# Performance work log

Hardware: AMD Instinct MI355X
Metric: run time of the kernel (lower is better)

## Reference

```python
import jax, jax.numpy as jnp
import numpy as np

B, D, L, H, P, IMG = 32, 768, 12, 12, 16, 224
N = (IMG // P) ** 2  # 196 patches
DH = D // H
FF = 4 * D
EPS = 1e-5


def _ln(x, w, b):
    m = jnp.mean(x, axis=-1, keepdims=True)
    v = jnp.mean((x - m) ** 2, axis=-1, keepdims=True)
    return (x - m) * jax.lax.rsqrt(v + EPS) * w + b


def setup_inputs() -> dict:
    key = jax.random.key(0)
    ks = jax.random.split(key, 12)
    s = 0.02
    return {
        "x": jax.random.normal(ks[0], (B, 3, IMG, IMG), jnp.float32),
        "patch_w": jax.random.normal(ks[1], (D, 3, P, P), jnp.float32) * s,
        "patch_b": jnp.zeros((D,), jnp.float32),
        "pos_embed": jax.random.normal(ks[2], (1, N, D), jnp.float32) * s,
        "ln1_w": jnp.ones((L, D), jnp.float32),
        "ln1_b": jnp.zeros((L, D), jnp.float32),
        "qkv_w": jax.random.normal(ks[3], (L, 3 * D, D), jnp.float32) * s,
        "qkv_b": jnp.zeros((L, 3 * D), jnp.float32),
        "proj_w": jax.random.normal(ks[4], (L, D, D), jnp.float32) * s,
        "proj_b": jnp.zeros((L, D), jnp.float32),
        "ln2_w": jnp.ones((L, D), jnp.float32),
        "ln2_b": jnp.zeros((L, D), jnp.float32),
        "fc1_w": jax.random.normal(ks[5], (L, FF, D), jnp.float32) * s,
        "fc1_b": jnp.zeros((L, FF), jnp.float32),
        "fc2_w": jax.random.normal(ks[6], (L, D, FF), jnp.float32) * s,
        "fc2_b": jnp.zeros((L, D), jnp.float32),
        "lnf_w": jnp.ones((D,), jnp.float32),
        "lnf_b": jnp.zeros((D,), jnp.float32),
    }


def reference(x, patch_w, patch_b, pos_embed, ln1_w, ln1_b, qkv_w, qkv_b,
              proj_w, proj_b, ln2_w, ln2_b, fc1_w, fc1_b, fc2_w, fc2_b,
              lnf_w, lnf_b):
    # Patch embed: strided conv, NCHW / OIHW
    h = jax.lax.conv_general_dilated(
        x, patch_w, window_strides=(P, P), padding="VALID",
        dimension_numbers=("NCHW", "OIHW", "NCHW")) + patch_b[None, :, None, None]
    b = h.shape[0]
    h = h.reshape(b, D, -1).transpose(0, 2, 1)  # (B, N, D)
    h = h + pos_embed  # broadcast over batch

    scale = DH ** (-0.5)
    for i in range(L):
        # --- attention (indices=None path: plain masked-free softmax) ---
        y = _ln(h, ln1_w[i], ln1_b[i])
        qkv = y @ qkv_w[i].T + qkv_b[i]                      # (B, N, 3D)
        qkv = qkv.reshape(b, -1, 3, H, DH).transpose(2, 0, 3, 1, 4)
        q, k, v = qkv[0], qkv[1], qkv[2]                     # (B, H, N, DH)
        attn = jax.nn.softmax(jnp.einsum("bhnd,bhmd->bhnm", q, k) * scale, axis=-1)
        o = jnp.einsum("bhnm,bhmd->bhnd", attn, v)
        o = o.transpose(0, 2, 1, 3).reshape(b, -1, D)
        h = h + (o @ proj_w[i].T + proj_b[i])
        # --- MLP ---
        y = _ln(h, ln2_w[i], ln2_b[i])
        y = jax.nn.gelu(y @ fc1_w[i].T + fc1_b[i], approximate=False)
        h = h + (y @ fc2_w[i].T + fc2_b[i])

    return _ln(h, lnf_w, lnf_b)
```

## Files before the change

kernel.cpp:

```cpp
#include <hip/hip_runtime.h>
#include <hip/hip_bf16.h>
#include <math.h>

#define BB    32
#define DD    768
#define LL    12
#define HH    12
#define NN    196
#define DHH   64
#define FFF   3072
#define MM    (BB * NN)
#define BHH   (BB * HH)

typedef float  floatx4 __attribute__((ext_vector_type(4)));
typedef __bf16 bf16x8  __attribute__((ext_vector_type(8)));

#define DEV __device__ __forceinline__

DEV unsigned short bf16u(float v) {
  __hip_bfloat16 h = __float2bfloat16(v);
  return __builtin_bit_cast(unsigned short, h);
}

DEV floatx4 mfma_bf16(bf16x8 a, bf16x8 b, floatx4 c) {
  return __builtin_amdgcn_mfma_f32_16x16x32_bf16(a, b, c, 0, 0, 0);
}

DEV void gl2lds16(const void* g, void* l) {
  __builtin_amdgcn_global_load_lds(
      (const __attribute__((address_space(1))) void*)g,
      (__attribute__((address_space(3))) void*)l, 16, 0, 0);
}

__global__ __launch_bounds__(256) void cvt4_k(const float4* __restrict__ in,
                                              ushort4* __restrict__ out, int n4) {
  int i = blockIdx.x * 256 + threadIdx.x;
  if (i < n4) {
    float4 v = in[i];
    ushort4 o;
    o.x = bf16u(v.x); o.y = bf16u(v.y); o.z = bf16u(v.z); o.w = bf16u(v.w);
    out[i] = o;
  }
}

__global__ __launch_bounds__(256) void im2col_k(const float* __restrict__ x,
                                                unsigned short* __restrict__ A) {
  int idx = blockIdx.x * 256 + threadIdx.x;
  int col = idx % DD;
  int token = idx / DD;
  int b = token / NN, p = token % NN;
  int pr = p / 14, pc = p % 14;
  int c = col >> 8, rm = col & 255, i = rm >> 4, j = rm & 15;
  float v = x[(((size_t)b * 3 + c) * 224 + pr * 16 + i) * 224 + pc * 16 + j];
  A[idx] = bf16u(v);
}

template <int F32OUT>
__global__ __launch_bounds__(256) void ln_k(const float* __restrict__ x,
                                            const float* __restrict__ w,
                                            const float* __restrict__ bb,
                                            void* __restrict__ outp) {
  const int token = blockIdx.x, tid = threadIdx.x;
  const float* xr = x + (size_t)token * DD;
  float v0 = xr[tid], v1 = xr[tid + 256], v2 = xr[tid + 512];
  float s = v0 + v1 + v2;
  float ss = v0 * v0 + v1 * v1 + v2 * v2;
#pragma unroll
  for (int off = 32; off; off >>= 1) {
    s += __shfl_down(s, off);
    ss += __shfl_down(ss, off);
  }
  __shared__ float rs[4], rq[4];
  if ((tid & 63) == 0) { rs[tid >> 6] = s; rq[tid >> 6] = ss; }
  __syncthreads();
  float tot = rs[0] + rs[1] + rs[2] + rs[3];
  float tq  = rq[0] + rq[1] + rq[2] + rq[3];
  const float mean = tot * (1.0f / 768.0f);
  const float var  = tq * (1.0f / 768.0f) - mean * mean;
  const float rstd = rsqrtf(var + 1e-5f);
#pragma unroll
  for (int t = 0; t < 3; t++) {
    int col = tid + t * 256;
    float xv = (t == 0) ? v0 : (t == 1 ? v1 : v2);
    float yv = (xv - mean) * rstd * w[col] + bb[col];
    if (F32OUT) ((float*)outp)[(size_t)token * DD + col] = yv;
    else        ((unsigned short*)outp)[(size_t)token * DD + col] = bf16u(yv);
  }
}


template <int MODE>
__global__ __launch_bounds__(256, 4) void gemm_bt(
    const unsigned short* __restrict__ A, const unsigned short* __restrict__ W,
    const float* __restrict__ bias, void* __restrict__ outp, int K, int Nn) {
  __shared__ unsigned short As[2][128 * 32];
  __shared__ unsigned short Bs[2][128 * 32];
  const int tid = threadIdx.x;
  const int wave = tid >> 6, lane = tid & 63;
  const int tm = blockIdx.y * 128, tn = blockIdx.x * 128;
  const int wm = (wave >> 1) * 64, wn = (wave & 1) * 64;
  const int lr = lane & 15, kq = lane >> 4;
  const int sw = (lr >> 1) & 3;
  const int koff = (kq ^ sw) * 8;
  const int c0 = tid, c1 = tid + 256;
  const int r0 = c0 >> 2, r1 = c1 >> 2;
  const int kc0 = ((c0 & 3) ^ ((r0 >> 1) & 3)) * 8;
  const int kc1 = ((c1 & 3) ^ ((r1 >> 1) & 3)) * 8;
  const size_t ga0 = (size_t)(tm + r0) * K + kc0;
  const size_t ga1 = (size_t)(tm + r1) * K + kc1;
  const size_t gb0 = (size_t)(tn + r0) * K + kc0;
  const size_t gb1 = (size_t)(tn + r1) * K + kc1;
  floatx4 acc[4][4] = {};
  auto stage = [&](int buf, int k0) {
    gl2lds16(A + ga0 + k0, &As[buf][c0 * 8]);
    gl2lds16(A + ga1 + k0, &As[buf][c1 * 8]);
    gl2lds16(W + gb0 + k0, &Bs[buf][c0 * 8]);
    gl2lds16(W + gb1 + k0, &Bs[buf][c1 * 8]);
  };
  const int nk = K >> 5;
  stage(0, 0);
  for (int it = 0; it < nk; it++) {
    const int cur = it & 1;
    __syncthreads();
    if (it + 1 < nk) stage(cur ^ 1, (it + 1) << 5);
    bf16x8 af[4], bq[4];
#pragma unroll
    for (int mi = 0; mi < 4; mi++)
      af[mi] = *(const bf16x8*)&As[cur][(wm + mi * 16 + lr) * 32 + koff];
#pragma unroll
    for (int ni = 0; ni < 4; ni++)
      bq[ni] = *(const bf16x8*)&Bs[cur][(wn + ni * 16 + lr) * 32 + koff];
#pragma unroll
    for (int mi = 0; mi < 4; mi++)
#pragma unroll
      for (int ni = 0; ni < 4; ni++)
        acc[mi][ni] = mfma_bf16(af[mi], bq[ni], acc[mi][ni]);
  }
  const int rbase = tm + wm + (lane >> 4) * 4;
  const int cbase = tn + wn + lr;
#pragma unroll
  for (int ni = 0; ni < 4; ni++) {
    const int col = cbase + ni * 16;
    const float bv = bias[col];
#pragma unroll
    for (int mi = 0; mi < 4; mi++) {
#pragma unroll
      for (int r = 0; r < 4; r++) {
        const int row = rbase + mi * 16 + r;
        float v = acc[mi][ni][r] + bv;
        if (MODE == 0) {
          ((unsigned short*)outp)[(size_t)row * Nn + col] = bf16u(v);
        } else {
          float g = 0.5f * v * (1.0f + erff(v * 0.70710678118654752f));
          ((unsigned short*)outp)[(size_t)row * Nn + col] = bf16u(g);
        }
      }
    }
  }
}

template <int MODE>
__global__ __launch_bounds__(256, 4) void gemm64_bt(
    const unsigned short* __restrict__ A, const unsigned short* __restrict__ W,
    const float* __restrict__ bias, const float* __restrict__ aux,
    float* __restrict__ outp, int K, int Nn) {
  __shared__ unsigned short As[2][64 * 32];
  __shared__ unsigned short Bs[2][128 * 32];
  const int tid = threadIdx.x;
  const int wave = tid >> 6, lane = tid & 63;
  const int tm = blockIdx.y * 64, tn = blockIdx.x * 128;
  const int wm = (wave >> 1) * 32, wn = (wave & 1) * 64;
  const int lr = lane & 15, kq = lane >> 4;
  const int sw = (lr >> 1) & 3;
  const int koff = (kq ^ sw) * 8;
  const int ra = tid >> 2;
  const int kca = ((tid & 3) ^ ((ra >> 1) & 3)) * 8;
  const int c0 = tid, c1 = tid + 256;
  const int r0 = c0 >> 2, r1 = c1 >> 2;
  const int kc0 = ((c0 & 3) ^ ((r0 >> 1) & 3)) * 8;
  const int kc1 = ((c1 & 3) ^ ((r1 >> 1) & 3)) * 8;
  const size_t ga  = (size_t)(tm + ra) * K + kca;
  const size_t gb0 = (size_t)(tn + r0) * K + kc0;
  const size_t gb1 = (size_t)(tn + r1) * K + kc1;
  floatx4 acc[2][4] = {};
  auto stage = [&](int buf, int k0) {
    gl2lds16(A + ga + k0, &As[buf][tid * 8]);
    gl2lds16(W + gb0 + k0, &Bs[buf][c0 * 8]);
    gl2lds16(W + gb1 + k0, &Bs[buf][c1 * 8]);
  };
  const int nk = K >> 5;
  stage(0, 0);
  for (int it = 0; it < nk; it++) {
    const int cur = it & 1;
    __syncthreads();
    if (it + 1 < nk) stage(cur ^ 1, (it + 1) << 5);
    bf16x8 af[2], bq[4];
#pragma unroll
    for (int mi = 0; mi < 2; mi++)
      af[mi] = *(const bf16x8*)&As[cur][(wm + mi * 16 + lr) * 32 + koff];
#pragma unroll
    for (int ni = 0; ni < 4; ni++)
      bq[ni] = *(const bf16x8*)&Bs[cur][(wn + ni * 16 + lr) * 32 + koff];
#pragma unroll
    for (int mi = 0; mi < 2; mi++)
#pragma unroll
      for (int ni = 0; ni < 4; ni++)
        acc[mi][ni] = mfma_bf16(af[mi], bq[ni], acc[mi][ni]);
  }
  const int rbase = tm + wm + (lane >> 4) * 4;
  const int cbase = tn + wn + lr;
#pragma unroll
  for (int ni = 0; ni < 4; ni++) {
    const int col = cbase + ni * 16;
    const float bv = bias[col];
#pragma unroll
    for (int mi = 0; mi < 2; mi++) {
#pragma unroll
      for (int r = 0; r < 4; r++) {
        const int row = rbase + mi * 16 + r;
        float v = acc[mi][ni][r] + bv;
        float* hp = outp + (size_t)row * Nn + col;
        if (MODE == 1) *hp = v + aux[(size_t)(row % NN) * Nn + col];
        else           *hp = *hp + v;
      }
    }
  }
}

__global__ __launch_bounds__(256) void attn_sm_k(const unsigned short* __restrict__ qkv,
                                                 unsigned short* __restrict__ P) {
  __shared__ float S[32][232];
  const int tid = threadIdx.x;
  const int bh = blockIdx.x;
  const int b = bh / HH, hh = bh % HH;
  const int i0 = blockIdx.y * 32;
  const int wave = tid >> 6, lane = tid & 63;
  const int lr = lane & 15, k8 = (lane >> 4) * 8;
  for (int t = wave; t < 28; t += 4) {
    const int til = (t / 14) * 16, tj = (t % 14) * 16;
    const int iq = min(i0 + til + lr, NN - 1), jk = min(tj + lr, NN - 1);
    const unsigned short* qb = qkv + (size_t)(b * NN + iq) * 2304 + hh * 64 + k8;
    const unsigned short* kb = qkv + (size_t)(b * NN + jk) * 2304 + 768 + hh * 64 + k8;
    floatx4 acc = {0.f, 0.f, 0.f, 0.f};
    acc = mfma_bf16(*(const bf16x8*)qb, *(const bf16x8*)kb, acc);
    acc = mfma_bf16(*(const bf16x8*)(qb + 32), *(const bf16x8*)(kb + 32), acc);
#pragma unroll
    for (int r = 0; r < 4; r++)
      S[til + (lane >> 4) * 4 + r][tj + lr] = acc[r] * 0.125f;
  }
  __syncthreads();
  const int row = tid >> 3, sub = tid & 7;
  float v[28];
  float m = -1e30f;
#pragma unroll
  for (int t = 0; t < 28; t++) {
    const int c = sub + t * 8;
    v[t] = (c < NN) ? S[row][c] : -1e30f;
    m = fmaxf(m, v[t]);
  }
  m = fmaxf(m, __shfl_xor(m, 1));
  m = fmaxf(m, __shfl_xor(m, 2));
  m = fmaxf(m, __shfl_xor(m, 4));
  float s = 0.f;
#pragma unroll
  for (int t = 0; t < 28; t++) {
    v[t] = (sub + t * 8 < NN) ? __expf(v[t] - m) : 0.f;
    s += v[t];
  }
  s += __shfl_xor(s, 1);
  s += __shfl_xor(s, 2);
  s += __shfl_xor(s, 4);
  const float inv = 1.0f / s;
  const int gi = i0 + row;
  if (gi < NN) {
    unsigned short* prow = P + ((size_t)bh * NN + gi) * 224;
#pragma unroll
    for (int t = 0; t < 28; t++) prow[sub + t * 8] = bf16u(v[t] * inv);
  }
}

__global__ __launch_bounds__(256) void vt_k(const unsigned short* __restrict__ qkv,
                                            unsigned short* __restrict__ Vt) {
  int idx = blockIdx.x * 256 + threadIdx.x;
  int j = idx % 224;
  int rest = idx / 224;
  int d = rest % 64, bh = rest / 64;
  int b = bh / HH, hh = bh % HH;
  unsigned short val = 0;
  if (j < NN) val = qkv[(size_t)(b * NN + j) * 2304 + 1536 + hh * 64 + d];
  Vt[idx] = val;
}

__global__ __launch_bounds__(256) void pv_k(const unsigned short* __restrict__ P,
                                            const unsigned short* __restrict__ Vt,
                                            unsigned short* __restrict__ o) {
  const int bh = blockIdx.x;
  const int b = bh / HH, hh = bh % HH;
  const int t = blockIdx.y * 4 + (threadIdx.x >> 6);
  const int it = t >> 2, dt = t & 3;
  const int lane = threadIdx.x & 63, lr = lane & 15, k8 = (lane >> 4) * 8;
  const int ip = min(it * 16 + lr, NN - 1);
  const unsigned short* pb = P + ((size_t)bh * NN + ip) * 224 + k8;
  const unsigned short* vb = Vt + ((size_t)bh * 64 + dt * 16 + lr) * 224 + k8;
  floatx4 acc = {0.f, 0.f, 0.f, 0.f};
#pragma unroll
  for (int k0 = 0; k0 < 224; k0 += 32)
    acc = mfma_bf16(*(const bf16x8*)(pb + k0), *(const bf16x8*)(vb + k0), acc);
#pragma unroll
  for (int r = 0; r < 4; r++) {
    int i = it * 16 + (lane >> 4) * 4 + r;
    if (i < NN)
      o[(size_t)(b * NN + i) * DD + hh * 64 + dt * 16 + lr] = bf16u(acc[r]);
  }
}

extern "C" void kernel_launch(void* const* d_in, const int* in_sizes, int n_in,
                              void* d_out, int out_size, void* d_ws, size_t ws_size,
                              hipStream_t stream) {
  const float* x       = (const float*)d_in[0];
  const float* patchw  = (const float*)d_in[1];
  const float* patchb  = (const float*)d_in[2];
  const float* pos     = (const float*)d_in[3];
  const float* ln1w    = (const float*)d_in[4];
  const float* ln1b    = (const float*)d_in[5];
  const float* qkvw    = (const float*)d_in[6];
  const float* qkvb    = (const float*)d_in[7];
  const float* projw   = (const float*)d_in[8];
  const float* projb   = (const float*)d_in[9];
  const float* ln2w    = (const float*)d_in[10];
  const float* ln2b    = (const float*)d_in[11];
  const float* fc1w    = (const float*)d_in[12];
  const float* fc1b    = (const float*)d_in[13];
  const float* fc2w    = (const float*)d_in[14];
  const float* fc2b    = (const float*)d_in[15];
  const float* lnfw    = (const float*)d_in[16];
  const float* lnfb    = (const float*)d_in[17];

  char* base = (char*)d_ws;
  size_t off = 0;
  auto alloc = [&](size_t bytes) {
    void* p = base + off;
    off = (off + bytes + 255) & ~(size_t)255;
    return p;
  };
  unsigned short* Wq  = (unsigned short*)alloc((size_t)LL * 2304 * 768 * 2);
  unsigned short* Wp  = (unsigned short*)alloc((size_t)LL * 768 * 768 * 2);
  unsigned short* W1  = (unsigned short*)alloc((size_t)LL * 3072 * 768 * 2);
  unsigned short* W2  = (unsigned short*)alloc((size_t)LL * 768 * 3072 * 2);
  unsigned short* Wpe = (unsigned short*)alloc((size_t)768 * 768 * 2);
  float*          h   = (float*)alloc((size_t)MM * DD * 4);
  unsigned short* y   = (unsigned short*)alloc((size_t)MM * DD * 2);
  unsigned short* qkv = (unsigned short*)alloc((size_t)MM * 2304 * 2);
  unsigned short* g   = (unsigned short*)alloc((size_t)MM * FFF * 2);
  unsigned short* P   = (unsigned short*)alloc((size_t)BHH * NN * 224 * 2);
  unsigned short* Vt  = (unsigned short*)alloc((size_t)BHH * 64 * 224 * 2);
  unsigned short* o   = (unsigned short*)alloc((size_t)MM * DD * 2);
  if (off > ws_size) return;

  unsigned short* Aim = qkv;

  auto cvt = [&](const float* src, unsigned short* dst, size_t n) {
    int n4 = (int)(n / 4);
    cvt4_k<<<dim3((n4 + 255) / 256), dim3(256), 0, stream>>>(
        (const float4*)src, (ushort4*)dst, n4);
  };
  cvt(qkvw, Wq, (size_t)LL * 2304 * 768);
  cvt(projw, Wp, (size_t)LL * 768 * 768);
  cvt(fc1w, W1, (size_t)LL * 3072 * 768);
  cvt(fc2w, W2, (size_t)LL * 768 * 3072);
  cvt(patchw, Wpe, (size_t)768 * 768);

  im2col_k<<<dim3(MM * DD / 256), dim3(256), 0, stream>>>(x, Aim);
  gemm64_bt<1><<<dim3(6, 98), dim3(256), 0, stream>>>(Aim, Wpe, patchb, pos, h, 768, 768);

  for (int l = 0; l < LL; l++) {
    ln_k<0><<<dim3(MM), dim3(256), 0, stream>>>(h, ln1w + l * 768, ln1b + l * 768, y);
    gemm_bt<0><<<dim3(18, 49), dim3(256), 0, stream>>>(
        y, Wq + (size_t)l * 2304 * 768, qkvb + l * 2304, qkv, 768, 2304);
    attn_sm_k<<<dim3(BHH, 7), dim3(256), 0, stream>>>(qkv, P);
    vt_k<<<dim3(BHH * 64 * 224 / 256), dim3(256), 0, stream>>>(qkv, Vt);
    pv_k<<<dim3(BHH, 13), dim3(256), 0, stream>>>(P, Vt, o);
    gemm64_bt<2><<<dim3(6, 98), dim3(256), 0, stream>>>(
        o, Wp + (size_t)l * 768 * 768, projb + l * 768, nullptr, h, 768, 768);
    ln_k<0><<<dim3(MM), dim3(256), 0, stream>>>(h, ln2w + l * 768, ln2b + l * 768, y);
    gemm_bt<3><<<dim3(24, 49), dim3(256), 0, stream>>>(
        y, W1 + (size_t)l * 3072 * 768, fc1b + l * 3072, g, 768, 3072);
    gemm64_bt<2><<<dim3(6, 98), dim3(256), 0, stream>>>(
        g, W2 + (size_t)l * 768 * 3072, fc2b + l * 768, nullptr, h, 3072, 768);
  }
  ln_k<1><<<dim3(MM), dim3(256), 0, stream>>>(h, lnfw, lnfb, d_out);
}
```

Before: 3.919 ms.

## Split-K proj/fc2 GEMMs into partial buffers and fuse residual add into LayerNorm

Replaces the 64-row residual-accumulating GEMM for the attention projection and fc2 with a 128x128-tile split-K GEMM (K halved over blockIdx.z). Each half writes fp32 partials to scratch buffers that reuse the qkv and P regions. A new LayerNorm kernel adds the two partials into the residual stream, writes it back, and produces the normalized bf16 output, also serving as the final LN. The aim is more MFMA reuse per tile and fewer separate residual/LN passes, at the cost of writing and reading two fp32 partial tensors.

```diff
diff --git a/kernel.cpp b/kernel.cpp
--- a/kernel.cpp
+++ b/kernel.cpp
@@ -55,11 +55,10 @@
   A[idx] = bf16u(v);
 }
 
-template <int F32OUT>
 __global__ __launch_bounds__(256) void ln_k(const float* __restrict__ x,
                                             const float* __restrict__ w,
                                             const float* __restrict__ bb,
-                                            void* __restrict__ outp) {
+                                            unsigned short* __restrict__ outp) {
   const int token = blockIdx.x, tid = threadIdx.x;
   const float* xr = x + (size_t)token * DD;
   float v0 = xr[tid], v1 = xr[tid + 256], v2 = xr[tid + 512];
@@ -83,8 +82,45 @@
     int col = tid + t * 256;
     float xv = (t == 0) ? v0 : (t == 1 ? v1 : v2);
     float yv = (xv - mean) * rstd * w[col] + bb[col];
-    if (F32OUT) ((float*)outp)[(size_t)token * DD + col] = yv;
-    else        ((unsigned short*)outp)[(size_t)token * DD + col] = bf16u(yv);
+    outp[(size_t)token * DD + col] = bf16u(yv);
+  }
+}
+
+template <int FINAL>
+__global__ __launch_bounds__(256) void ln_fuse_k(float* __restrict__ h,
+    const float* __restrict__ p0, const float* __restrict__ p1,
+    const float* __restrict__ w, const float* __restrict__ bb,
+    void* __restrict__ outp) {
+  const int token = blockIdx.x, tid = threadIdx.x;
+  const size_t base = (size_t)token * DD;
+  float v[3];
+#pragma unroll
+  for (int t = 0; t < 3; t++) {
+    const int col = tid + t * 256;
+    v[t] = h[base + col] + p0[base + col] + p1[base + col];
+    if (!FINAL) h[base + col] = v[t];
+  }
+  float s = v[0] + v[1] + v[2];
+  float ss = v[0] * v[0] + v[1] * v[1] + v[2] * v[2];
+#pragma unroll
+  for (int off = 32; off; off >>= 1) {
+    s += __shfl_down(s, off);
+    ss += __shfl_down(ss, off);
+  }
+  __shared__ float rs[4], rq[4];
+  if ((tid & 63) == 0) { rs[tid >> 6] = s; rq[tid >> 6] = ss; }
+  __syncthreads();
+  float tot = rs[0] + rs[1] + rs[2] + rs[3];
+  float tq  = rq[0] + rq[1] + rq[2] + rq[3];
+  const float mean = tot * (1.0f / 768.0f);
+  const float var  = tq * (1.0f / 768.0f) - mean * mean;
+  const float rstd = rsqrtf(var + 1e-5f);
+#pragma unroll
+  for (int t = 0; t < 3; t++) {
+    const int col = tid + t * 256;
+    float yv = (v[t] - mean) * rstd * w[col] + bb[col];
+    if (FINAL) ((float*)outp)[base + col] = yv;
+    else       ((unsigned short*)outp)[base + col] = bf16u(yv);
   }
 }
 
@@ -154,6 +190,74 @@
           float g = 0.5f * v * (1.0f + erff(v * 0.70710678118654752f));
           ((unsigned short*)outp)[(size_t)row * Nn + col] = bf16u(g);
         }
+      }
+    }
+  }
+}
+
+__global__ __launch_bounds__(256, 4) void gemm_sk(
+    const unsigned short* __restrict__ A, const unsigned short* __restrict__ W,
+    const float* __restrict__ bias, float* __restrict__ p0,
+    float* __restrict__ p1, int K, int Nn) {
+  __shared__ unsigned short As[2][128 * 32];
+  __shared__ unsigned short Bs[2][128 * 32];
+  const int tid = threadIdx.x;
+  const int wave = tid >> 6, lane = tid & 63;
+  const int tm = blockIdx.y * 128, tn = blockIdx.x * 128;
+  const int kz = blockIdx.z;
+  const int kper = K >> 1;
+  const int kbase = kz * kper;
+  const int wm = (wave >> 1) * 64, wn = (wave & 1) * 64;
+  const int lr = lane & 15, kq = lane >> 4;
+  const int sw = (lr >> 1) & 3;
+  const int koff = (kq ^ sw) * 8;
+  const int c0 = tid, c1 = tid + 256;
+  const int r0 = c0 >> 2, r1 = c1 >> 2;
+  const int kc0 = ((c0 & 3) ^ ((r0 >> 1) & 3)) * 8;
+  const int kc1 = ((c1 & 3) ^ ((r1 >> 1) & 3)) * 8;
+  const size_t ga0 = (size_t)(tm + r0) * K + kc0 + kbase;
+  const size_t ga1 = (size_t)(tm + r1) * K + kc1 + kbase;
+  const size_t gb0 = (size_t)(tn + r0) * K + kc0 + kbase;
+  const size_t gb1 = (size_t)(tn + r1) * K + kc1 + kbase;
+  floatx4 acc[4][4] = {};
+  auto stage = [&](int buf, int k0) {
+    gl2lds16(A + ga0 + k0, &As[buf][c0 * 8]);
+    gl2lds16(A + ga1 + k0, &As[buf][c1 * 8]);
+    gl2lds16(W + gb0 + k0, &Bs[buf][c0 * 8]);
+    gl2lds16(W + gb1 + k0, &Bs[buf][c1 * 8]);
+  };
+  const int nk = kper >> 5;
+  stage(0, 0);
+  for (int it = 0; it < nk; it++) {
+    const int cur = it & 1;
+    __syncthreads();
+    if (it + 1 < nk) stage(cur ^ 1, (it + 1) << 5);
+    bf16x8 af[4], bq[4];
+#pragma unroll
+    for (int mi = 0; mi < 4; mi++)
+      af[mi] = *(const bf16x8*)&As[cur][(wm + mi * 16 + lr) * 32 + koff];
+#pragma unroll
+    for (int ni = 0; ni < 4; ni++)
+      bq[ni] = *(const bf16x8*)&Bs[cur][(wn + ni * 16 + lr) * 32 + koff];
+#pragma unroll
+    for (int mi = 0; mi < 4; mi++)
+#pragma unroll
+      for (int ni = 0; ni < 4; ni++)
+        acc[mi][ni] = mfma_bf16(af[mi], bq[ni], acc[mi][ni]);
+  }
+  float* __restrict__ po = kz ? p1 : p0;
+  const int rbase = tm + wm + (lane >> 4) * 4;
+  const int cbase = tn + wn + lr;
+#pragma unroll
+  for (int ni = 0; ni < 4; ni++) {
+    const int col = cbase + ni * 16;
+    const float bv = kz ? 0.0f : bias[col];
+#pragma unroll
+    for (int mi = 0; mi < 4; mi++) {
+#pragma unroll
+      for (int r = 0; r < 4; r++) {
+        const int row = rbase + mi * 16 + r;
+        po[(size_t)row * Nn + col] = acc[mi][ni][r] + bv;
       }
     }
   }
@@ -358,6 +462,8 @@
   if (off > ws_size) return;
 
   unsigned short* Aim = qkv;
+  float* pp0 = (float*)qkv;
+  float* pp1 = (float*)P;
 
   auto cvt = [&](const float* src, unsigned short* dst, size_t n) {
     int n4 = (int)(n / 4);
@@ -373,20 +479,28 @@
   im2col_k<<<dim3(MM * DD / 256), dim3(256), 0, stream>>>(x, Aim);
   gemm64_bt<1><<<dim3(6, 98), dim3(256), 0, stream>>>(Aim, Wpe, patchb, pos, h, 768, 768);
 
+  ln_k<<<dim3(MM), dim3(256), 0, stream>>>(h, ln1w, ln1b, y);
+
   for (int l = 0; l < LL; l++) {
-    ln_k<0><<<dim3(MM), dim3(256), 0, stream>>>(h, ln1w + l * 768, ln1b + l * 768, y);
     gemm_bt<0><<<dim3(18, 49), dim3(256), 0, stream>>>(
         y, Wq + (size_t)l * 2304 * 768, qkvb + l * 2304, qkv, 768, 2304);
     attn_sm_k<<<dim3(BHH, 7), dim3(256), 0, stream>>>(qkv, P);
     vt_k<<<dim3(BHH * 64 * 224 / 256), dim3(256), 0, stream>>>(qkv, Vt);
     pv_k<<<dim3(BHH, 13), dim3(256), 0, stream>>>(P, Vt, o);
-    gemm64_bt<2><<<dim3(6, 98), dim3(256), 0, stream>>>(
-        o, Wp + (size_t)l * 768 * 768, projb + l * 768, nullptr, h, 768, 768);
-    ln_k<0><<<dim3(MM), dim3(256), 0, stream>>>(h, ln2w + l * 768, ln2b + l * 768, y);
+    gemm_sk<<<dim3(6, 49, 2), dim3(256), 0, stream>>>(
+        o, Wp + (size_t)l * 768 * 768, projb + l * 768, pp0, pp1, 768, 768);
+    ln_fuse_k<0><<<dim3(MM), dim3(256), 0, stream>>>(
+        h, pp0, pp1, ln2w + l * 768, ln2b + l * 768, y);
     gemm_bt<3><<<dim3(24, 49), dim3(256), 0, stream>>>(
         y, W1 + (size_t)l * 3072 * 768, fc1b + l * 3072, g, 768, 3072);
-    gemm64_bt<2><<<dim3(6, 98), dim3(256), 0, stream>>>(
-        g, W2 + (size_t)l * 768 * 3072, fc2b + l * 768, nullptr, h, 3072, 768);
-  }
-  ln_k<1><<<dim3(MM), dim3(256), 0, stream>>>(h, lnfw, lnfb, d_out);
-}
+    gemm_sk<<<dim3(6, 49, 2), dim3(256), 0, stream>>>(
+        g, W2 + (size_t)l * 768 * 3072, fc2b + l * 768, pp0, pp1, 3072, 768);
+    if (l + 1 < LL) {
+      ln_fuse_k<0><<<dim3(MM), dim3(256), 0, stream>>>(
+          h, pp0, pp1, ln1w + (l + 1) * 768, ln1b + (l + 1) * 768, y);
+    } else {
+      ln_fuse_k<1><<<dim3(MM), dim3(256), 0, stream>>>(
+          h, pp0, pp1, lnfw, lnfb, d_out);
+    }
+  }
+}
```

Result: faster. 3.788 ms (-3.3%).
